# Optimization experiments

Measured on AMD Instinct MI355X. Metric: run time of the kernel, lower is better.

## Reference

```python
import jax, jax.numpy as jnp
import numpy as np

B, S, D, H = 4, 2048, 1024, 16
HD = D // H
THETA = 10000.0


def rope(x, pos, theta=THETA):
    # x: [..., seq, d], pos: broadcastable to [..., seq]
    d = x.shape[-1]
    half = d // 2
    inv_freq = 1.0 / (theta ** (jnp.arange(half, dtype=jnp.float32) * 2.0 / d))  # [half]
    ang = pos[..., None].astype(jnp.float32) * inv_freq  # [..., seq, half]
    cos, sin = jnp.cos(ang), jnp.sin(ang)
    x1, x2 = x[..., 0::2], x[..., 1::2]
    r1 = x1 * cos - x2 * sin
    r2 = x1 * sin + x2 * cos
    return jnp.stack([r1, r2], axis=-1).reshape(x.shape).astype(x.dtype)


def setup_inputs() -> dict:
    key = jax.random.key(0)
    ks = jax.random.split(key, 5)
    x = jax.random.normal(ks[0], (B, S, D), dtype=jnp.float32)
    token_positions = jnp.tile(jnp.arange(S, dtype=jnp.int64 if jax.config.jax_enable_x64 else jnp.int32), (B, 1))
    scale = 0.02
    Wq = jax.random.normal(ks[1], (D, D), dtype=jnp.float32) * scale
    Wk = jax.random.normal(ks[2], (D, D), dtype=jnp.float32) * scale
    Wv = jax.random.normal(ks[3], (D, D), dtype=jnp.float32) * scale
    Wo = jax.random.normal(ks[4], (D, D), dtype=jnp.float32) * scale
    return {"x": x, "token_positions": token_positions, "Wq": Wq, "Wk": Wk, "Wv": Wv, "Wo": Wo}


def reference(x, token_positions, Wq, Wk, Wv, Wo):
    b, s, d = x.shape
    # QKV projections (torch Linear: x @ W.T), split heads -> [b, h, s, hd]
    def proj(W):
        y = jnp.einsum('bsd,ed->bse', x, W)
        return y.reshape(b, s, H, HD).transpose(0, 2, 1, 3)
    Q, K, V = proj(Wq), proj(Wk), proj(Wv)
    # token_positions [..., seq] -> [..., 1, seq] to broadcast over heads
    pos = token_positions[:, None, :]  # [b, 1, s]
    Q = rope(Q, pos)
    K = rope(K, pos)
    # causal mask and scaled dot-product attention
    idx = jnp.arange(s)
    causal = idx[:, None] >= idx[None, :]  # [s, s], query >= key
    scores = jnp.einsum('bhqd,bhkd->bhqk', Q, K) / jnp.sqrt(jnp.float32(HD))
    scores = jnp.where(causal, scores, -jnp.inf)
    weights = jax.nn.softmax(scores, axis=-1)
    o = jnp.einsum('bhqk,bhkd->bhqd', weights, V)
    o = o.transpose(0, 2, 1, 3).reshape(b, s, d)  # merge heads
    return jnp.einsum('bsd,ed->bse', o, Wo)
```

## Files before the change

kernel.cpp:

```cpp
#include <hip/hip_runtime.h>

#define S_LEN 2048
#define NH 16
#define HDIM 64
#define DMODEL 1024

typedef __attribute__((ext_vector_type(8))) short bf16x8;
typedef __attribute__((ext_vector_type(4))) float f32x4;

__device__ __forceinline__ short f2bf(float f) {
    union { float f; unsigned u; } x; x.f = f;
    unsigned r = x.u + 0x7fffu + ((x.u >> 16) & 1u);
    return (short)(r >> 16);
}

#define GLDS(g, l) __builtin_amdgcn_global_load_lds( \
    (__attribute__((address_space(1))) void*)(g),    \
    (__attribute__((address_space(3))) void*)(l), 16, 0, 0)

#define QSCALE 0.18033688011112042f
#define FREQ_L 0.41524101186109327f

__global__ __launch_bounds__(256) void prep(const float* __restrict__ x,
                                            const float* __restrict__ wq,
                                            const float* __restrict__ wk,
                                            const float* __restrict__ wv,
                                            const float* __restrict__ wo,
                                            const int* __restrict__ tp,
                                            short* __restrict__ xb,
                                            short* __restrict__ wqb,
                                            short* __restrict__ wkb,
                                            short* __restrict__ wvb,
                                            short* __restrict__ wob,
                                            float2* __restrict__ tab) {
    int bid = blockIdx.x;
    if (bid < 8192) {
        int i = bid * 256 + threadIdx.x;
        float4 v = ((const float4*)x)[i];
        short4 o;
        o.x = f2bf(v.x); o.y = f2bf(v.y); o.z = f2bf(v.z); o.w = f2bf(v.w);
        ((short4*)xb)[i] = o;
    } else if (bid < 12288) {
        int sel = (bid - 8192) >> 10;
        const float* in = sel == 0 ? wq : sel == 1 ? wk : sel == 2 ? wv : wo;
        short* out = sel == 0 ? wqb : sel == 1 ? wkb : sel == 2 ? wvb : wob;
        int i = ((bid - 8192) & 1023) * 256 + threadIdx.x;
        float4 v = ((const float4*)in)[i];
        short4 o;
        o.x = f2bf(v.x); o.y = f2bf(v.y); o.z = f2bf(v.z); o.w = f2bf(v.w);
        ((short4*)out)[i] = o;
    } else {
        int idx = (bid - 12288) * 256 + threadIdx.x;
        int b = idx >> 16, s = (idx >> 5) & 2047, i = idx & 31;
        float p = (float)tp[(b << 11) + s];
        float freq = exp2f(-(float)i * FREQ_L);
        float sn, cs;
        sincosf(p * freq, &sn, &cs);
        tab[idx] = make_float2(cs, sn);
    }
}

__global__ __launch_bounds__(512) void gemm_qkv(const short* __restrict__ A,
                                                const short* __restrict__ Bq,
                                                const short* __restrict__ Bk,
                                                const short* __restrict__ Bv,
                                                const float2* __restrict__ tab,
                                                short* __restrict__ Qo,
                                                short* __restrict__ Ko,
                                                short* __restrict__ Vo) {
    constexpr int K = 1024;
    __shared__ __align__(16) short smem[3 * 24576];

    const int sel = blockIdx.x >> 3;
    const int bn = blockIdx.x & 7;
    const int bm = blockIdx.y;
    const short* Bm = sel == 0 ? Bq : sel == 1 ? Bk : Bv;
    short* Cb = sel == 0 ? Qo : sel == 1 ? Ko : Vo;

    const int tid = threadIdx.x;
    const int lane = tid & 63;
    const int w = tid >> 6;
    const int wm = w >> 1;
    const int wn = w & 1;
    const int quad = lane >> 4, l16 = lane & 15;
    const int l7 = l16 & 7;

    int aoff[4], boff[2];
#pragma unroll
    for (int i = 0; i < 4; i++) {
        int Lc = i * 512 + tid;
        int row = Lc >> 3;
        int cc = (Lc & 7) ^ (row & 7);
        aoff[i] = (bm * 256 + row) * K + cc * 8;
    }
#pragma unroll
    for (int i = 0; i < 2; i++) {
        int Lc = i * 512 + tid;
        int row = Lc >> 3;
        int cc = (Lc & 7) ^ (row & 7);
        boff[i] = (bn * 128 + row) * K + cc * 8;
    }

    auto stage = [&](int h, int slot) {
        char* sbase = (char*)smem + slot * 49152;
        const int kh = h * 64;
#pragma unroll
        for (int i = 0; i < 4; i++)
            GLDS(A + aoff[i] + kh, sbase + i * 8192 + w * 1024);
#pragma unroll
        for (int i = 0; i < 2; i++)
            GLDS(Bm + boff[i] + kh, sbase + 32768 + i * 8192 + w * 1024);
    };

    f32x4 acc[4][4] = {};

    auto compute = [&](int slot) {
        const short* sA = smem + slot * 24576;
        const short* sB = sA + 16384;
#pragma unroll
        for (int kc = 0; kc < 2; kc++) {
            const int c = ((kc * 4 + quad) ^ l7) * 8;
            bf16x8 af[4], bfm[4];
#pragma unroll
            for (int mi = 0; mi < 4; mi++)
                af[mi] = *(const bf16x8*)&sA[(wm * 64 + mi * 16 + l16) * 64 + c];
#pragma unroll
            for (int ni = 0; ni < 4; ni++)
                bfm[ni] = *(const bf16x8*)&sB[(wn * 64 + ni * 16 + l16) * 64 + c];
            __builtin_amdgcn_s_setprio(1);
#pragma unroll
            for (int mi = 0; mi < 4; mi++)
#pragma unroll
                for (int ni = 0; ni < 4; ni++)
                    acc[mi][ni] = __builtin_amdgcn_mfma_f32_16x16x32_bf16(af[mi], bfm[ni],
                                                                          acc[mi][ni], 0, 0, 0);
            __builtin_amdgcn_s_setprio(0);
        }
    };

    stage(0, 0); stage(1, 1);

    auto step = [&](int h, int sc, int ss) {
        asm volatile("s_waitcnt vmcnt(6)" ::: "memory");
        __builtin_amdgcn_s_barrier();
        __builtin_amdgcn_sched_barrier(0);
        stage(h + 2, ss);
        compute(sc);
    };

    for (int h = 0; h < 12; h += 3) {
        step(h + 0, 0, 2);
        step(h + 1, 1, 0);
        step(h + 2, 2, 1);
    }
    step(12, 0, 2);
    step(13, 1, 0);
    asm volatile("s_waitcnt vmcnt(6)" ::: "memory");
    __builtin_amdgcn_s_barrier();
    __builtin_amdgcn_sched_barrier(0);
    compute(2);
    asm volatile("s_waitcnt vmcnt(0)" ::: "memory");
    __builtin_amdgcn_s_barrier();
    __builtin_amdgcn_sched_barrier(0);
    compute(0);

    const int gm0 = bm * 256 + wm * 64;
    const int gn0 = bn * 128 + wn * 64;

    if (sel == 2) {
        short* T = smem;
        __syncthreads();
#pragma unroll
        for (int mi = 0; mi < 4; mi++) {
            int lmb = wm * 64 + mi * 16 + quad * 4;
#pragma unroll
            for (int ni = 0; ni < 4; ni++) {
                int ln = wn * 64 + ni * 16 + l16;
                short4 pk;
                pk.x = f2bf(acc[mi][ni][0]);
                pk.y = f2bf(acc[mi][ni][1]);
                pk.z = f2bf(acc[mi][ni][2]);
                pk.w = f2bf(acc[mi][ni][3]);
                *(short4*)&T[ln * 256 + (lmb ^ ((ln & 31) << 3))] = pk;
            }
        }
        __syncthreads();
        const int row = tid >> 2, qt = tid & 3;
        const int grow = bn * 128 + row;
        const int gb = bm >> 3;
        const int gs0 = (bm & 7) * 256;
        short* dst = Cb + (((size_t)(gb * NH + (grow >> 6)) * HDIM + (grow & 63)) * S_LEN
                           + gs0 + qt * 64);
#pragma unroll
        for (int j = 0; j < 8; j++) {
            bf16x8 v = *(const bf16x8*)&T[row * 256 +
                        ((qt * 64 + j * 8) ^ ((row & 31) << 3))];
            *(bf16x8*)(dst + j * 8) = v;
        }
    } else {
        const float qs = (sel == 0) ? QSCALE : 1.0f;
#pragma unroll
        for (int mi = 0; mi < 4; mi++)
#pragma unroll
            for (int r = 0; r < 4; r++) {
                int gm = gm0 + mi * 16 + quad * 4 + r;
                const float2* trow = tab + (gm << 5);
                int b = gm >> 11, s = gm & 2047;
#pragma unroll
                for (int ni = 0; ni < 4; ni++) {
                    float2 cs = trow[ni * 8 + (l16 >> 1)];
                    float v = acc[mi][ni][r];
                    float prt = __shfl_xor(v, 1, 64);
                    float val = (l16 & 1) ? (prt * cs.y + v * cs.x)
                                          : (v * cs.x - prt * cs.y);
                    int gn = gn0 + ni * 16 + l16;
                    int h = gn >> 6, hd = gn & 63;
                    Cb[((b * NH + h) * S_LEN + s) * HDIM + hd] = f2bf(val * qs);
                }
            }
    }
}

__global__ __launch_bounds__(256) void gemm_o(const short* __restrict__ A,
                                              const short* __restrict__ Bw,
                                              float* __restrict__ Cf) {
    constexpr int N = 1024, K = 1024, BK = 32;
    __shared__ __align__(16) short sa[3][128 * BK];
    __shared__ __align__(16) short sb[3][64 * BK];

    const int tid = threadIdx.x;
    const int lane = tid & 63;
    const int w = tid >> 6;
    const int quad = lane >> 4, l16 = lane & 15;
    const int bn = blockIdx.x, bm = blockIdx.y;
    const int arow0 = bm * 128, brow0 = bn * 64;

    int aoff[2], boff;
#pragma unroll
    for (int i = 0; i < 2; i++) {
        int cs = i * 256 + tid;
        int row = cs >> 2;
        int gc = (cs & 3) ^ ((row >> 1) & 3);
        aoff[i] = (arow0 + row) * K + gc * 8;
    }
    {
        int row = tid >> 2;
        int gc = (tid & 3) ^ ((row >> 1) & 3);
        boff = (brow0 + row) * K + gc * 8;
    }

    auto stage = [&](int kt, int b) {
        const int k0 = kt * BK;
#pragma unroll
        for (int i = 0; i < 2; i++)
            GLDS(A + aoff[i] + k0, (char*)&sa[b][0] + i * 4096 + w * 1024);
        GLDS(Bw + boff + k0, (char*)&sb[b][0] + w * 1024);
    };

    f32x4 acc[2][4] = {};
    const int rsw = (quad ^ ((l16 >> 1) & 3)) * 8;

    auto compute = [&](int b) {
        bf16x8 af[2];
#pragma unroll
        for (int mi = 0; mi < 2; mi++)
            af[mi] = *(const bf16x8*)&sa[b][(w * 32 + mi * 16 + l16) * BK + rsw];
#pragma unroll
        for (int ni = 0; ni < 4; ni++) {
            bf16x8 bfr = *(const bf16x8*)&sb[b][(ni * 16 + l16) * BK + rsw];
#pragma unroll
            for (int mi = 0; mi < 2; mi++)
                acc[mi][ni] = __builtin_amdgcn_mfma_f32_16x16x32_bf16(af[mi], bfr,
                                                                     acc[mi][ni], 0, 0, 0);
        }
    };

    stage(0, 0);
    stage(1, 1);

    auto step = [&](int kt, int b, int bs) {
        asm volatile("s_waitcnt vmcnt(3)" ::: "memory");
        __builtin_amdgcn_s_barrier();
        __builtin_amdgcn_sched_barrier(0);
        stage(kt + 2, bs);
        compute(b);
    };

    for (int kt = 0; kt < 30; kt += 3) {
        step(kt + 0, 0, 2);
        step(kt + 1, 1, 0);
        step(kt + 2, 2, 1);
    }
    asm volatile("s_waitcnt vmcnt(3)" ::: "memory");
    __builtin_amdgcn_s_barrier();
    __builtin_amdgcn_sched_barrier(0);
    compute(0);
    asm volatile("s_waitcnt vmcnt(0)" ::: "memory");
    __builtin_amdgcn_s_barrier();
    __builtin_amdgcn_sched_barrier(0);
    compute(1);

    const int gm0 = arow0 + w * 32;
#pragma unroll
    for (int mi = 0; mi < 2; mi++)
#pragma unroll
        for (int ni = 0; ni < 4; ni++)
#pragma unroll
            for (int r = 0; r < 4; r++) {
                int gm = gm0 + mi * 16 + quad * 4 + r;
                int gn = brow0 + ni * 16 + l16;
                Cf[gm * N + gn] = acc[mi][ni][r];
            }
}

__global__ __launch_bounds__(256, 3) void attn(const short* __restrict__ Q,
                                               const short* __restrict__ Km,
                                               const short* __restrict__ Vt,
                                               short* __restrict__ O) {
    __shared__ __align__(16) short kbuf[2][64 * 64];
    __shared__ __align__(16) short vbuf[2][64 * 64];
    __shared__ __align__(16) short pbuf[4][32 * 64];

    const int lane = threadIdx.x & 63;
    const int w = threadIdx.x >> 6;
    const int quad = lane >> 4, l16 = lane & 15;
    const int l7 = l16 & 7;
    const int bh = blockIdx.y;

    const short* Qg = Q  + bh * S_LEN * 64;
    const short* Kg = Km + bh * S_LEN * 64;
    const short* Vg = Vt + bh * 64 * S_LEN;
    short* myp = &pbuf[w][0];

    const int b = bh >> 4, h = bh & 15;

    bf16x8 ones;
#pragma unroll
    for (int j = 0; j < 8; j++) ones[j] = (short)0x3f80;

    auto stage = [&](int kt, int par) {
        const short* kt_base = Kg + kt * 64 * 64;
        const short* vt_base = Vg + kt * 64;
#pragma unroll
        for (int i = 0; i < 2; ++i) {
            int ch = w * 128 + i * 64 + lane;
            int row = ch >> 3;
            int c = (ch & 7) ^ (row & 7);
            GLDS(kt_base + row * 64 + c * 8, (char*)&kbuf[par][(w * 128 + i * 64) * 8]);
        }
#pragma unroll
        for (int i = 0; i < 2; ++i) {
            int ch = w * 128 + i * 64 + lane;
            int row = ch >> 3;
            int c = (ch & 7) ^ (row & 7);
            GLDS(vt_base + row * S_LEN + c * 8, (char*)&vbuf[par][(w * 128 + i * 64) * 8]);
        }
    };

    const int QtA = blockIdx.x;
    const int QtB = 15 - blockIdx.x;

    stage(0, 0);
    int t = 0;

    for (int phase = 0; phase < 2; ++phase) {
        const int Qt = phase ? QtB : QtA;
        const int nkt = 2 * Qt + 2;

        bf16x8 aq[2][2];
#pragma unroll
        for (int mi = 0; mi < 2; mi++) {
            int qrow = Qt * 128 + w * 32 + mi * 16 + l16;
#pragma unroll
            for (int kc = 0; kc < 2; kc++)
                aq[mi][kc] = *(const bf16x8*)&Qg[qrow * 64 + kc * 32 + quad * 8];
        }

        f32x4 oacc[2][4] = {};
        f32x4 lacc[2] = {};

        for (int kt = 0; kt < nkt; ++kt, ++t) {
            __syncthreads();
            if (kt + 1 < nkt)    stage(kt + 1, (t + 1) & 1);
            else if (phase == 0) stage(0,      (t + 1) & 1);
            const short* kb_cur = &kbuf[t & 1][0];
            const short* vb_cur = &vbuf[t & 1][0];

            f32x4 sc[2][4] = {};
            __builtin_amdgcn_s_setprio(1);
#pragma unroll
            for (int nt = 0; nt < 4; nt++) {
                int raddr = (nt * 16 + l16) * 64;
#pragma unroll
                for (int kc = 0; kc < 2; kc++) {
                    bf16x8 kf = *(const bf16x8*)&kb_cur[raddr + (((quad + kc * 4) ^ l7) * 8)];
                    sc[0][nt] = __builtin_amdgcn_mfma_f32_16x16x32_bf16(aq[0][kc], kf, sc[0][nt], 0, 0, 0);
                    sc[1][nt] = __builtin_amdgcn_mfma_f32_16x16x32_bf16(aq[1][kc], kf, sc[1][nt], 0, 0, 0);
                }
            }
            __builtin_amdgcn_s_setprio(0);
            if (kt >= nkt - 2) {
#pragma unroll
                for (int mi = 0; mi < 2; mi++)
#pragma unroll
                    for (int nt = 0; nt < 4; nt++)
#pragma unroll
                        for (int r = 0; r < 4; r++) {
                            int col = kt * 64 + nt * 16 + l16;
                            int row = Qt * 128 + w * 32 + mi * 16 + quad * 4 + r;
                            if (col > row) sc[mi][nt][r] = -__builtin_inff();
                        }
            }
#pragma unroll
            for (int mi = 0; mi < 2; mi++)
#pragma unroll
                for (int nt = 0; nt < 4; nt++)
#pragma unroll
                    for (int r = 0; r < 4; r++) {
                        float pv = __builtin_amdgcn_exp2f(sc[mi][nt][r]);
                        int q = mi * 16 + quad * 4 + r;
                        union { float f; unsigned short us[2]; } uu;
                        uu.f = pv;
                        myp[q * 64 + (((nt * 2 + (l16 >> 3)) ^ (q & 7)) * 8) + l7] =
                            (short)uu.us[1];
                    }
            bf16x8 ap[2][2];
#pragma unroll
            for (int mi = 0; mi < 2; mi++)
#pragma unroll
                for (int kc = 0; kc < 2; kc++)
                    ap[mi][kc] = *(const bf16x8*)&myp[(mi * 16 + l16) * 64 +
                                                      (((quad + kc * 4) ^ l7) * 8)];
            __builtin_amdgcn_s_setprio(1);
#pragma unroll
            for (int nt = 0; nt < 4; nt++) {
                int raddr = (nt * 16 + l16) * 64;
#pragma unroll
                for (int kc = 0; kc < 2; kc++) {
                    bf16x8 vf = *(const bf16x8*)&vb_cur[raddr + (((quad + kc * 4) ^ l7) * 8)];
                    oacc[0][nt] = __builtin_amdgcn_mfma_f32_16x16x32_bf16(ap[0][kc], vf, oacc[0][nt], 0, 0, 0);
                    oacc[1][nt] = __builtin_amdgcn_mfma_f32_16x16x32_bf16(ap[1][kc], vf, oacc[1][nt], 0, 0, 0);
                }
            }
#pragma unroll
            for (int mi = 0; mi < 2; mi++) {
                lacc[mi] = __builtin_amdgcn_mfma_f32_16x16x32_bf16(ap[mi][0], ones, lacc[mi], 0, 0, 0);
                lacc[mi] = __builtin_amdgcn_mfma_f32_16x16x32_bf16(ap[mi][1], ones, lacc[mi], 0, 0, 0);
            }
            __builtin_amdgcn_s_setprio(0);
        }
#pragma unroll
        for (int mi = 0; mi < 2; mi++)
#pragma unroll
            for (int r = 0; r < 4; r++) {
                float inv = 1.0f / lacc[mi][r];
                int srow = Qt * 128 + w * 32 + mi * 16 + quad * 4 + r;
#pragma unroll
                for (int nt = 0; nt < 4; nt++) {
                    int hd = nt * 16 + l16;
                    O[(b * S_LEN + srow) * DMODEL + h * HDIM + hd] = f2bf(oacc[mi][nt][r] * inv);
                }
            }
    }
}

extern "C" void kernel_launch(void* const* d_in, const int* in_sizes, int n_in,
                              void* d_out, int out_size, void* d_ws, size_t ws_size,
                              hipStream_t stream) {
    const float* x  = (const float*)d_in[0];
    const int*   tp = (const int*)d_in[1];
    const float* Wq = (const float*)d_in[2];
    const float* Wk = (const float*)d_in[3];
    const float* Wv = (const float*)d_in[4];
    const float* Wo = (const float*)d_in[5];
    float* out = (float*)d_out;

    char* ws = (char*)d_ws;
    const size_t MB = 1024 * 1024;
    short* xb  = (short*)(ws);
    short* wqb = (short*)(ws + 16 * MB);
    short* wkb = (short*)(ws + 18 * MB);
    short* wvb = (short*)(ws + 20 * MB);
    short* wob = (short*)(ws + 22 * MB);
    short* Qb  = (short*)(ws + 24 * MB);
    short* Kb  = (short*)(ws + 40 * MB);
    short* Vtb = (short*)(ws + 56 * MB);
    float2* tab = (float2*)d_out;

    prep<<<13312, 256, 0, stream>>>(x, Wq, Wk, Wv, Wo, tp,
                                    xb, wqb, wkb, wvb, wob, tab);

    gemm_qkv<<<dim3(24, 32), 512, 0, stream>>>(xb, wqb, wkb, wvb, tab, Qb, Kb, Vtb);

    attn<<<dim3(8, 64), 256, 0, stream>>>(Qb, Kb, Vtb, xb);

    gemm_o<<<dim3(16, 64), 256, 0, stream>>>(xb, wob, out);
}
```

Measured before the change: 248.0 us.

## Software-pipeline attention loop: overlap QK of tile k with PV of tile k-1

Restructures the attention inner loop so that the QK^T MFMAs for the current key tile are issued alongside the PV MFMAs for the previous tile. Exp and P-writes then overlap with matrix work. K/V shared buffers go from double to triple buffering so the previous V tile stays resident, and the loop is unrolled by two with ping-pong P register fragments. The extra LDS and registers push launch bounds down from 3 to 2 blocks per SM, which lowers occupancy.

```diff
diff --git a/kernel.cpp b/kernel.cpp
--- a/kernel.cpp
+++ b/kernel.cpp
@@ -313,12 +313,12 @@
             }
 }
 
-__global__ __launch_bounds__(256, 3) void attn(const short* __restrict__ Q,
+__global__ __launch_bounds__(256, 2) void attn(const short* __restrict__ Q,
                                                const short* __restrict__ Km,
                                                const short* __restrict__ Vt,
                                                short* __restrict__ O) {
-    __shared__ __align__(16) short kbuf[2][64 * 64];
-    __shared__ __align__(16) short vbuf[2][64 * 64];
+    __shared__ __align__(16) short kbuf[3][64 * 64];
+    __shared__ __align__(16) short vbuf[3][64 * 64];
     __shared__ __align__(16) short pbuf[4][32 * 64];
 
     const int lane = threadIdx.x & 63;
@@ -338,7 +338,7 @@
 #pragma unroll
     for (int j = 0; j < 8; j++) ones[j] = (short)0x3f80;
 
-    auto stage = [&](int kt, int par) {
+    auto stage = [&](int kt, int slot) {
         const short* kt_base = Kg + kt * 64 * 64;
         const short* vt_base = Vg + kt * 64;
 #pragma unroll
@@ -346,22 +346,23 @@
             int ch = w * 128 + i * 64 + lane;
             int row = ch >> 3;
             int c = (ch & 7) ^ (row & 7);
-            GLDS(kt_base + row * 64 + c * 8, (char*)&kbuf[par][(w * 128 + i * 64) * 8]);
+            GLDS(kt_base + row * 64 + c * 8, (char*)&kbuf[slot][(w * 128 + i * 64) * 8]);
         }
 #pragma unroll
         for (int i = 0; i < 2; ++i) {
             int ch = w * 128 + i * 64 + lane;
             int row = ch >> 3;
             int c = (ch & 7) ^ (row & 7);
-            GLDS(vt_base + row * S_LEN + c * 8, (char*)&vbuf[par][(w * 128 + i * 64) * 8]);
+            GLDS(vt_base + row * S_LEN + c * 8, (char*)&vbuf[slot][(w * 128 + i * 64) * 8]);
         }
     };
 
     const int QtA = blockIdx.x;
     const int QtB = 15 - blockIdx.x;
 
+    bf16x8 apA[2][2], apB[2][2];
+    int s0 = 0;
     stage(0, 0);
-    int t = 0;
 
     for (int phase = 0; phase < 2; ++phase) {
         const int Qt = phase ? QtB : QtA;
@@ -379,12 +380,14 @@
         f32x4 oacc[2][4] = {};
         f32x4 lacc[2] = {};
 
-        for (int kt = 0; kt < nkt; ++kt, ++t) {
+        auto iter = [&](int kt, int scur, int snext, int sprev,
+                        bf16x8 (&apc)[2][2], bf16x8 (&app)[2][2], bool hasPrev) {
             __syncthreads();
-            if (kt + 1 < nkt)    stage(kt + 1, (t + 1) & 1);
-            else if (phase == 0) stage(0,      (t + 1) & 1);
-            const short* kb_cur = &kbuf[t & 1][0];
-            const short* vb_cur = &vbuf[t & 1][0];
+            int stk = kt + 1;
+            if (stk < nkt)       stage(stk, snext);
+            else if (phase == 0) stage(0,   snext);
+            const short* kb = &kbuf[scur][0];
+            const short* vb = &vbuf[sprev][0];
 
             f32x4 sc[2][4] = {};
             __builtin_amdgcn_s_setprio(1);
@@ -393,12 +396,30 @@
                 int raddr = (nt * 16 + l16) * 64;
 #pragma unroll
                 for (int kc = 0; kc < 2; kc++) {
-                    bf16x8 kf = *(const bf16x8*)&kb_cur[raddr + (((quad + kc * 4) ^ l7) * 8)];
+                    bf16x8 kf = *(const bf16x8*)&kb[raddr + (((quad + kc * 4) ^ l7) * 8)];
                     sc[0][nt] = __builtin_amdgcn_mfma_f32_16x16x32_bf16(aq[0][kc], kf, sc[0][nt], 0, 0, 0);
                     sc[1][nt] = __builtin_amdgcn_mfma_f32_16x16x32_bf16(aq[1][kc], kf, sc[1][nt], 0, 0, 0);
                 }
             }
+            if (hasPrev) {
+#pragma unroll
+                for (int nt = 0; nt < 4; nt++) {
+                    int raddr = (nt * 16 + l16) * 64;
+#pragma unroll
+                    for (int kc = 0; kc < 2; kc++) {
+                        bf16x8 vf = *(const bf16x8*)&vb[raddr + (((quad + kc * 4) ^ l7) * 8)];
+                        oacc[0][nt] = __builtin_amdgcn_mfma_f32_16x16x32_bf16(app[0][kc], vf, oacc[0][nt], 0, 0, 0);
+                        oacc[1][nt] = __builtin_amdgcn_mfma_f32_16x16x32_bf16(app[1][kc], vf, oacc[1][nt], 0, 0, 0);
+                    }
+                }
+#pragma unroll
+                for (int mi = 0; mi < 2; mi++) {
+                    lacc[mi] = __builtin_amdgcn_mfma_f32_16x16x32_bf16(app[mi][0], ones, lacc[mi], 0, 0, 0);
+                    lacc[mi] = __builtin_amdgcn_mfma_f32_16x16x32_bf16(app[mi][1], ones, lacc[mi], 0, 0, 0);
+                }
+            }
             __builtin_amdgcn_s_setprio(0);
+
             if (kt >= nkt - 2) {
 #pragma unroll
                 for (int mi = 0; mi < 2; mi++)
@@ -424,28 +445,39 @@
                         myp[q * 64 + (((nt * 2 + (l16 >> 3)) ^ (q & 7)) * 8) + l7] =
                             (short)uu.us[1];
                     }
-            bf16x8 ap[2][2];
 #pragma unroll
             for (int mi = 0; mi < 2; mi++)
 #pragma unroll
                 for (int kc = 0; kc < 2; kc++)
-                    ap[mi][kc] = *(const bf16x8*)&myp[(mi * 16 + l16) * 64 +
-                                                      (((quad + kc * 4) ^ l7) * 8)];
+                    apc[mi][kc] = *(const bf16x8*)&myp[(mi * 16 + l16) * 64 +
+                                                       (((quad + kc * 4) ^ l7) * 8)];
+        };
+
+        for (int kt = 0; kt < nkt; kt += 2) {
+            int s1 = s0 + 1; if (s1 == 3) s1 = 0;
+            int s2 = s1 + 1; if (s2 == 3) s2 = 0;
+            iter(kt,     s0, s1, s2, apA, apB, kt > 0);
+            iter(kt + 1, s1, s2, s0, apB, apA, true);
+            s0 = s2;
+        }
+        {
+            int slast = s0 - 1; if (slast < 0) slast = 2;
+            const short* vb = &vbuf[slast][0];
             __builtin_amdgcn_s_setprio(1);
 #pragma unroll
             for (int nt = 0; nt < 4; nt++) {
                 int raddr = (nt * 16 + l16) * 64;
 #pragma unroll
                 for (int kc = 0; kc < 2; kc++) {
-                    bf16x8 vf = *(const bf16x8*)&vb_cur[raddr + (((quad + kc * 4) ^ l7) * 8)];
-                    oacc[0][nt] = __builtin_amdgcn_mfma_f32_16x16x32_bf16(ap[0][kc], vf, oacc[0][nt], 0, 0, 0);
-                    oacc[1][nt] = __builtin_amdgcn_mfma_f32_16x16x32_bf16(ap[1][kc], vf, oacc[1][nt], 0, 0, 0);
+                    bf16x8 vf = *(const bf16x8*)&vb[raddr + (((quad + kc * 4) ^ l7) * 8)];
+                    oacc[0][nt] = __builtin_amdgcn_mfma_f32_16x16x32_bf16(apB[0][kc], vf, oacc[0][nt], 0, 0, 0);
+                    oacc[1][nt] = __builtin_amdgcn_mfma_f32_16x16x32_bf16(apB[1][kc], vf, oacc[1][nt], 0, 0, 0);
                 }
             }
 #pragma unroll
             for (int mi = 0; mi < 2; mi++) {
-                lacc[mi] = __builtin_amdgcn_mfma_f32_16x16x32_bf16(ap[mi][0], ones, lacc[mi], 0, 0, 0);
-                lacc[mi] = __builtin_amdgcn_mfma_f32_16x16x32_bf16(ap[mi][1], ones, lacc[mi], 0, 0, 0);
+                lacc[mi] = __builtin_amdgcn_mfma_f32_16x16x32_bf16(apB[mi][0], ones, lacc[mi], 0, 0, 0);
+                lacc[mi] = __builtin_amdgcn_mfma_f32_16x16x32_bf16(apB[mi][1], ones, lacc[mi], 0, 0, 0);
             }
             __builtin_amdgcn_s_setprio(0);
         }
```

New measurement: 245.4 us. No clear change (-1.0%).
